# Kernel optimization log

Hardware: AMD Instinct MI355X
Metric: run time of the kernel (lower is better)

Reference implementation:

```python
import jax, jax.numpy as jnp
import numpy as np

NUM_CLASSES = 1000
FEAT_DIM = 512
BATCH = 16384


def setup_inputs() -> dict:
    key = jax.random.key(0)
    k1, k2, k3 = jax.random.split(key, 3)
    x = jax.random.normal(k1, (BATCH, FEAT_DIM), dtype=jnp.float32)
    labels = jax.random.randint(k2, (BATCH,), 0, NUM_CLASSES, dtype=jnp.int64)
    centers = jax.random.normal(k3, (NUM_CLASSES, FEAT_DIM), dtype=jnp.float32)
    margin = jnp.ones((1,), dtype=jnp.float32)
    return {"x": x, "labels": labels, "centers": centers, "margin": margin}


def reference(x, labels, centers, margin):
    # squared euclidean distances: [B, C]
    distmat = (
        jnp.sum(x * x, axis=1, keepdims=True)
        + jnp.sum(centers * centers, axis=1)[None, :]
        - 2.0 * (x @ centers.T)
    )
    B, C = distmat.shape
    onehot = labels[:, None] == jnp.arange(C, dtype=labels.dtype)[None, :]  # [B, C]
    # distance to the true-class center
    dist = jnp.sum(jnp.where(onehot, distmat, 0.0), axis=1)  # [B]
    # min distance over all other classes (mask true class with +inf)
    dist_min = jnp.min(jnp.where(onehot, jnp.inf, distmat), axis=1)  # [B]
    m = margin[0]
    loss = jnp.sum(jnp.maximum(m + dist - dist_min, 0.0)) / B
    return loss
```

## Files before the change

kernel.cpp:

```cpp
#include <hip/hip_runtime.h>
#include <hip/hip_bf16.h>

#define BATCH 16384
#define NCLS  1000
#define NPAD  1024
#define FDIM  512

#define CBLK_STRIDE 266240
#define TAIL_OFF    262144
#define XBLK_STRIDE 262144

typedef __bf16 bf16x8 __attribute__((ext_vector_type(8)));
typedef float  f32x16 __attribute__((ext_vector_type(16)));

#define GLOBAL_AS __attribute__((address_space(1)))
#define LDS_AS    __attribute__((address_space(3)))

#define VMCNT(n) asm volatile("s_waitcnt vmcnt(" #n ")" ::: "memory")
#define LGKM0()  asm volatile("s_waitcnt lgkmcnt(0)" ::: "memory")
#define SBAR()   __builtin_amdgcn_s_barrier()
#define SCHED0() __builtin_amdgcn_sched_barrier(0)

__global__ __launch_bounds__(256) void prep(
    const float* __restrict__ centers, const float* __restrict__ x,
    char* __restrict__ cbt, char* __restrict__ xbt, float* __restrict__ out)
{
    const int bid = blockIdx.x, t = threadIdx.x;
    if (bid == 0 && t == 0) out[0] = 0.f;

    if (bid < 256) {
        const int lane = t & 63;
        const int c = bid * 4 + (t >> 6);
        const int cblk = c >> 8, cl = c & 255;
        char* base = cbt + (size_t)cblk * CBLK_STRIDE;

        float4 f0 = make_float4(0.f, 0.f, 0.f, 0.f);
        float4 f1 = make_float4(0.f, 0.f, 0.f, 0.f);
        if (c < NCLS) {
            f0 = *(const float4*)(centers + (size_t)c * FDIM + lane * 8);
            f1 = *(const float4*)(centers + (size_t)c * FDIM + lane * 8 + 4);
        }
        bf16x8 b;
        b[0] = (__bf16)f0.x; b[1] = (__bf16)f0.y; b[2] = (__bf16)f0.z; b[3] = (__bf16)f0.w;
        b[4] = (__bf16)f1.x; b[5] = (__bf16)f1.y; b[6] = (__bf16)f1.z; b[7] = (__bf16)f1.w;
        *(bf16x8*)(base + (lane >> 3) * 32768 + (lane & 7) * 4096 + cl * 16) = b;

        float ssum = f0.x*f0.x + f0.y*f0.y + f0.z*f0.z + f0.w*f0.w
                   + f1.x*f1.x + f1.y*f1.y + f1.z*f1.z + f1.w*f1.w;
        #pragma unroll
        for (int o = 32; o > 0; o >>= 1) ssum += __shfl_down(ssum, o);
        if (lane == 0) {
            const float hf = (c < NCLS) ? (-0.5f * ssum) : -1e30f;
            const __bf16 h = (__bf16)hf;
            const __bf16 l = (c < NCLS) ? (__bf16)(hf - (float)h) : (__bf16)0.f;
            bf16x8 tl;
            #pragma unroll
            for (int e = 0; e < 8; ++e) tl[e] = (__bf16)0.f;
            tl[0] = h; tl[1] = l;
            *(bf16x8*)(base + TAIL_OFF + cl * 16) = tl;
        }
    } else {
        const int pid  = bid - 256;
        const int bblk = pid >> 3, s = pid & 7;
        const float* src = x + (size_t)(bblk * 256 + t) * FDIM + s * 64;
        float4 f[16];
        #pragma unroll
        for (int j = 0; j < 16; ++j) f[j] = *(const float4*)(src + j * 4);
        char* dst = xbt + (size_t)bblk * XBLK_STRIDE + s * 32768 + t * 16;
        #pragma unroll
        for (int c = 0; c < 8; ++c) {
            bf16x8 b;
            b[0] = (__bf16)f[c*2].x;   b[1] = (__bf16)f[c*2].y;
            b[2] = (__bf16)f[c*2].z;   b[3] = (__bf16)f[c*2].w;
            b[4] = (__bf16)f[c*2+1].x; b[5] = (__bf16)f[c*2+1].y;
            b[6] = (__bf16)f[c*2+1].z; b[7] = (__bf16)f[c*2+1].w;
            *(bf16x8*)(dst + c * 4096) = b;
        }
    }
}

__global__ __launch_bounds__(512, 1) void trip_main(
    const int* __restrict__ labels, const char* __restrict__ cbt,
    const char* __restrict__ xbt, float* __restrict__ mxp,
    float* __restrict__ dap)
{
    extern __shared__ char lds[];
    const int t    = threadIdx.x;
    const int lane = t & 63;
    const int w    = t >> 6;
    const int wN   = w & 3, wM = w >> 2;
    const int l31  = lane & 31, hi = lane >> 5;
    const int bid  = blockIdx.x;
    const int cblk = bid >> 6;
    const int bblk = bid & 63;
    const int class0 = cblk * 256;
    const int row0   = bblk * 256;
    const char* cbB  = cbt + (size_t)cblk * CBLK_STRIDE;
    const char* xbB  = xbt + (size_t)bblk * XBLK_STRIDE;

    auto stageU = [&](int T, int u) {
        const int boff = (T & 1) * 32768 + u * 8192 + t * 16;
        const int goff = T * 32768 + u * 8192 + t * 16;
        __builtin_amdgcn_global_load_lds((const GLOBAL_AS void*)(cbB + goff),
                                         (LDS_AS void*)(lds + boff), 16, 0, 0);
        __builtin_amdgcn_global_load_lds((const GLOBAL_AS void*)(xbB + goff),
                                         (LDS_AS void*)(lds + 65536 + boff), 16, 0, 0);
    };

    f32x16 acc[4][2];
    #pragma unroll
    for (int mi = 0; mi < 4; ++mi)
        #pragma unroll
        for (int ni = 0; ni < 2; ++ni)
            #pragma unroll
            for (int r = 0; r < 16; ++r) acc[mi][ni][r] = 0.f;

    const int lab0 = labels[row0 + wN * 64 + l31];
    const int lab1 = labels[row0 + wN * 64 + 32 + l31];
    SCHED0();
    if (t < 256) {
        const char* src = cbB + TAIL_OFF + t * 16;
        char* dst = lds + 131072 + t * 16;
        __builtin_amdgcn_global_load_lds((const GLOBAL_AS void*)src,
                                         (LDS_AS void*)dst, 16, 0, 0);
    }
    SCHED0();
    stageU(0, 0); SCHED0();
    stageU(0, 1); SCHED0();
    stageU(0, 2); SCHED0();
    stageU(0, 3);
    VMCNT(6);
    SBAR(); SCHED0();

    #pragma unroll
    for (int T = 0; T < 8; ++T) {
        const char* A = lds + (T & 1) * 32768;
        const char* B = lds + 65536 + (T & 1) * 32768;
        #pragma unroll
        for (int u = 0; u < 4; ++u) {
            if (T < 7)          VMCNT(4);
            else if (u == 0)    VMCNT(4);
            else if (u == 1)    VMCNT(2);
            else if (u == 2)    VMCNT(0);
            const int chunk = u * 2 + hi;
            bf16x8 a0 = *(const bf16x8*)(A + chunk * 4096 + (wM * 128 +  0 + l31) * 16);
            bf16x8 a1 = *(const bf16x8*)(A + chunk * 4096 + (wM * 128 + 32 + l31) * 16);
            bf16x8 a2 = *(const bf16x8*)(A + chunk * 4096 + (wM * 128 + 64 + l31) * 16);
            bf16x8 a3 = *(const bf16x8*)(A + chunk * 4096 + (wM * 128 + 96 + l31) * 16);
            bf16x8 b0 = *(const bf16x8*)(B + chunk * 4096 + (wN * 64 +  0 + l31) * 16);
            bf16x8 b1 = *(const bf16x8*)(B + chunk * 4096 + (wN * 64 + 32 + l31) * 16);
            if (T < 7) stageU(T + 1, u);
            SBAR();
            LGKM0();
            SCHED0();
            __builtin_amdgcn_s_setprio(1);
            acc[0][0] = __builtin_amdgcn_mfma_f32_32x32x16_bf16(a0, b0, acc[0][0], 0, 0, 0);
            acc[0][1] = __builtin_amdgcn_mfma_f32_32x32x16_bf16(a0, b1, acc[0][1], 0, 0, 0);
            acc[1][0] = __builtin_amdgcn_mfma_f32_32x32x16_bf16(a1, b0, acc[1][0], 0, 0, 0);
            acc[1][1] = __builtin_amdgcn_mfma_f32_32x32x16_bf16(a1, b1, acc[1][1], 0, 0, 0);
            acc[2][0] = __builtin_amdgcn_mfma_f32_32x32x16_bf16(a2, b0, acc[2][0], 0, 0, 0);
            acc[2][1] = __builtin_amdgcn_mfma_f32_32x32x16_bf16(a2, b1, acc[2][1], 0, 0, 0);
            acc[3][0] = __builtin_amdgcn_mfma_f32_32x32x16_bf16(a3, b0, acc[3][0], 0, 0, 0);
            acc[3][1] = __builtin_amdgcn_mfma_f32_32x32x16_bf16(a3, b1, acc[3][1], 0, 0, 0);
            __builtin_amdgcn_s_setprio(0);
            SBAR();
            SCHED0();
        }
    }

    {
        const char* T = lds + 131072;
        bf16x8 bt;
        #pragma unroll
        for (int e = 0; e < 8; ++e) bt[e] = (__bf16)0.f;
        if (hi == 0) { bt[0] = (__bf16)1.0f; bt[1] = (__bf16)1.0f; }
        #pragma unroll
        for (int mi = 0; mi < 4; ++mi) {
            bf16x8 a = *(const bf16x8*)(T + (wM * 128 + mi * 32 + l31) * 16);
            #pragma unroll
            for (int ni = 0; ni < 2; ++ni)
                acc[mi][ni] = __builtin_amdgcn_mfma_f32_32x32x16_bf16(
                    a, bt, acc[mi][ni], 0, 0, 0);
        }
    }

    const int labBase = class0 + wM * 128 + hi * 4;
    const int labA0 = lab0 - labBase;
    const int labA1 = lab1 - labBase;
    float MX0 = -3e38f, MX1 = -3e38f, DA0 = -3e38f, DA1 = -3e38f;
    #pragma unroll
    for (int mi = 0; mi < 4; ++mi) {
        #pragma unroll
        for (int r = 0; r < 16; ++r) {
            const int pat = mi * 32 + (r & 3) + 8 * (r >> 2);
            {
                const float a = acc[mi][0][r];
                const bool is = (labA0 == pat);
                MX0 = fmaxf(MX0, is ? -3e38f : a);
                DA0 = is ? a : DA0;
            }
            {
                const float a = acc[mi][1][r];
                const bool is = (labA1 == pat);
                MX1 = fmaxf(MX1, is ? -3e38f : a);
                DA1 = is ? a : DA1;
            }
        }
    }
    MX0 = fmaxf(MX0, __shfl_xor(MX0, 32));
    DA0 = fmaxf(DA0, __shfl_xor(DA0, 32));
    MX1 = fmaxf(MX1, __shfl_xor(MX1, 32));
    DA1 = fmaxf(DA1, __shfl_xor(DA1, 32));

    float* sc = (float*)lds;
    const int i0 = (wN * 2 + 0) * 32 + l31;
    const int i1 = (wN * 2 + 1) * 32 + l31;
    __syncthreads();
    if (wM == 1 && hi == 0) {
        sc[i0] = MX0; sc[256 + i0] = DA0;
        sc[i1] = MX1; sc[256 + i1] = DA1;
    }
    __syncthreads();
    if (wM == 0 && hi == 0) {
        const float M0 = fmaxf(MX0, sc[i0]),  D0 = fmaxf(DA0, sc[256 + i0]);
        const float M1 = fmaxf(MX1, sc[i1]),  D1 = fmaxf(DA1, sc[256 + i1]);
        const int rg = row0 + wN * 64 + l31;
        mxp[cblk * BATCH + rg]      = M0;
        dap[cblk * BATCH + rg]      = D0;
        mxp[cblk * BATCH + rg + 32] = M1;
        dap[cblk * BATCH + rg + 32] = D1;
    }
}

__global__ __launch_bounds__(256) void combine(
    const float* __restrict__ mxp, const float* __restrict__ dap,
    const float* __restrict__ margin, float* __restrict__ out)
{
    const int t = threadIdx.x;
    const int row = blockIdx.x * 256 + t;
    float mx = fmaxf(fmaxf(mxp[row], mxp[BATCH + row]),
                     fmaxf(mxp[2 * BATCH + row], mxp[3 * BATCH + row]));
    float da = fmaxf(fmaxf(dap[row], dap[BATCH + row]),
                     fmaxf(dap[2 * BATCH + row], dap[3 * BATCH + row]));
    float loss = fmaxf(margin[0] - 2.f * da + 2.f * mx, 0.f);
    __shared__ float red[4];
    #pragma unroll
    for (int o = 32; o > 0; o >>= 1) loss += __shfl_down(loss, o);
    if ((t & 63) == 0) red[t >> 6] = loss;
    __syncthreads();
    if (t == 0)
        atomicAdd(out, (red[0] + red[1] + red[2] + red[3]) * (1.0f / BATCH));
}

extern "C" void kernel_launch(void* const* d_in, const int* in_sizes, int n_in,
                              void* d_out, int out_size, void* d_ws, size_t ws_size,
                              hipStream_t stream)
{
    const float* x       = (const float*)d_in[0];
    const int*   labels  = (const int*)d_in[1];
    const float* centers = (const float*)d_in[2];
    const float* margin  = (const float*)d_in[3];
    float* out = (float*)d_out;

    char* ws = (char*)d_ws;
    char*  cbt  = ws;
    char*  xbt  = ws + 1064960;
    float* mxp  = (float*)(ws + 17842176);
    float* dap  = (float*)(ws + 18104320);

    (void)hipFuncSetAttribute((const void*)trip_main,
                              hipFuncAttributeMaxDynamicSharedMemorySize, 135168);

    prep<<<768, 256, 0, stream>>>(centers, x, cbt, xbt, out);
    trip_main<<<256, 512, 135168, stream>>>(labels, cbt, xbt, mxp, dap);
    combine<<<64, 256, 0, stream>>>(mxp, dap, margin, out);
}
```

Measured before the change: 33.24 us.

## Load x operand directly into registers, stage only centers through LDS

The x (B) tile is now read with direct global loads into double-buffered register arrays instead of being staged through LDS with global_load_lds. LDS usage roughly halves and the tail block moves down, which cuts LDS traffic and shared-memory footprint. It raises register pressure (16 extra bf16x8 vectors per thread) and changes the vmcnt accounting for the pipeline. Each wave now issues its own uncoalesced-ish global loads for B, and with 256 blocks of 512 threads occupancy likely stays one block per CU.

```diff
diff --git a/kernel.cpp b/kernel.cpp
--- a/kernel.cpp
+++ b/kernel.cpp
@@ -98,13 +98,11 @@
     const char* cbB  = cbt + (size_t)cblk * CBLK_STRIDE;
     const char* xbB  = xbt + (size_t)bblk * XBLK_STRIDE;
 
-    auto stageU = [&](int T, int u) {
-        const int boff = (T & 1) * 32768 + u * 8192 + t * 16;
-        const int goff = T * 32768 + u * 8192 + t * 16;
-        __builtin_amdgcn_global_load_lds((const GLOBAL_AS void*)(cbB + goff),
-                                         (LDS_AS void*)(lds + boff), 16, 0, 0);
-        __builtin_amdgcn_global_load_lds((const GLOBAL_AS void*)(xbB + goff),
-                                         (LDS_AS void*)(lds + 65536 + boff), 16, 0, 0);
+    auto stageAu = [&](int T, int u) {
+        const int off = u * 8192 + t * 16;
+        __builtin_amdgcn_global_load_lds(
+            (const GLOBAL_AS void*)(cbB + T * 32768 + off),
+            (LDS_AS void*)(lds + (T & 1) * 32768 + off), 16, 0, 0);
     };
 
     f32x16 acc[4][2];
@@ -115,53 +113,62 @@
             #pragma unroll
             for (int r = 0; r < 16; ++r) acc[mi][ni][r] = 0.f;
 
+    bf16x8 bE[4][2], bO[4][2];
+
     const int lab0 = labels[row0 + wN * 64 + l31];
     const int lab1 = labels[row0 + wN * 64 + 32 + l31];
-    SCHED0();
     if (t < 256) {
         const char* src = cbB + TAIL_OFF + t * 16;
-        char* dst = lds + 131072 + t * 16;
+        char* dst = lds + 65536 + t * 16;
         __builtin_amdgcn_global_load_lds((const GLOBAL_AS void*)src,
                                          (LDS_AS void*)dst, 16, 0, 0);
     }
-    SCHED0();
-    stageU(0, 0); SCHED0();
-    stageU(0, 1); SCHED0();
-    stageU(0, 2); SCHED0();
-    stageU(0, 3);
-    VMCNT(6);
+    #pragma unroll
+    for (int u = 0; u < 4; ++u) stageAu(0, u);
+    #pragma unroll
+    for (int u = 0; u < 4; ++u) {
+        const char* bsrc = xbB + (u * 2 + hi) * 4096 + (wN * 64 + l31) * 16;
+        bE[u][0] = *(const bf16x8*)(bsrc);
+        bE[u][1] = *(const bf16x8*)(bsrc + 512);
+    }
+    VMCNT(0);
     SBAR(); SCHED0();
 
     #pragma unroll
     for (int T = 0; T < 8; ++T) {
         const char* A = lds + (T & 1) * 32768;
-        const char* B = lds + 65536 + (T & 1) * 32768;
+        auto& bCur = (T & 1) ? bO : bE;
+        auto& bNxt = (T & 1) ? bE : bO;
         #pragma unroll
         for (int u = 0; u < 4; ++u) {
-            if (T < 7)          VMCNT(4);
-            else if (u == 0)    VMCNT(4);
-            else if (u == 1)    VMCNT(2);
-            else if (u == 2)    VMCNT(0);
+            if (T < 7)       { VMCNT(6); }
+            else if (u == 0) { VMCNT(6); }
+            else if (u == 1) { VMCNT(3); }
+            else if (u == 2) { VMCNT(0); }
             const int chunk = u * 2 + hi;
             bf16x8 a0 = *(const bf16x8*)(A + chunk * 4096 + (wM * 128 +  0 + l31) * 16);
             bf16x8 a1 = *(const bf16x8*)(A + chunk * 4096 + (wM * 128 + 32 + l31) * 16);
             bf16x8 a2 = *(const bf16x8*)(A + chunk * 4096 + (wM * 128 + 64 + l31) * 16);
             bf16x8 a3 = *(const bf16x8*)(A + chunk * 4096 + (wM * 128 + 96 + l31) * 16);
-            bf16x8 b0 = *(const bf16x8*)(B + chunk * 4096 + (wN * 64 +  0 + l31) * 16);
-            bf16x8 b1 = *(const bf16x8*)(B + chunk * 4096 + (wN * 64 + 32 + l31) * 16);
-            if (T < 7) stageU(T + 1, u);
+            if (T < 7) {
+                stageAu(T + 1, u);
+                const char* bsrc = xbB + (T + 1) * 32768 + chunk * 4096
+                                 + (wN * 64 + l31) * 16;
+                bNxt[u][0] = *(const bf16x8*)(bsrc);
+                bNxt[u][1] = *(const bf16x8*)(bsrc + 512);
+            }
             SBAR();
             LGKM0();
             SCHED0();
             __builtin_amdgcn_s_setprio(1);
-            acc[0][0] = __builtin_amdgcn_mfma_f32_32x32x16_bf16(a0, b0, acc[0][0], 0, 0, 0);
-            acc[0][1] = __builtin_amdgcn_mfma_f32_32x32x16_bf16(a0, b1, acc[0][1], 0, 0, 0);
-            acc[1][0] = __builtin_amdgcn_mfma_f32_32x32x16_bf16(a1, b0, acc[1][0], 0, 0, 0);
-            acc[1][1] = __builtin_amdgcn_mfma_f32_32x32x16_bf16(a1, b1, acc[1][1], 0, 0, 0);
-            acc[2][0] = __builtin_amdgcn_mfma_f32_32x32x16_bf16(a2, b0, acc[2][0], 0, 0, 0);
-            acc[2][1] = __builtin_amdgcn_mfma_f32_32x32x16_bf16(a2, b1, acc[2][1], 0, 0, 0);
-            acc[3][0] = __builtin_amdgcn_mfma_f32_32x32x16_bf16(a3, b0, acc[3][0], 0, 0, 0);
-            acc[3][1] = __builtin_amdgcn_mfma_f32_32x32x16_bf16(a3, b1, acc[3][1], 0, 0, 0);
+            acc[0][0] = __builtin_amdgcn_mfma_f32_32x32x16_bf16(a0, bCur[u][0], acc[0][0], 0, 0, 0);
+            acc[0][1] = __builtin_amdgcn_mfma_f32_32x32x16_bf16(a0, bCur[u][1], acc[0][1], 0, 0, 0);
+            acc[1][0] = __builtin_amdgcn_mfma_f32_32x32x16_bf16(a1, bCur[u][0], acc[1][0], 0, 0, 0);
+            acc[1][1] = __builtin_amdgcn_mfma_f32_32x32x16_bf16(a1, bCur[u][1], acc[1][1], 0, 0, 0);
+            acc[2][0] = __builtin_amdgcn_mfma_f32_32x32x16_bf16(a2, bCur[u][0], acc[2][0], 0, 0, 0);
+            acc[2][1] = __builtin_amdgcn_mfma_f32_32x32x16_bf16(a2, bCur[u][1], acc[2][1], 0, 0, 0);
+            acc[3][0] = __builtin_amdgcn_mfma_f32_32x32x16_bf16(a3, bCur[u][0], acc[3][0], 0, 0, 0);
+            acc[3][1] = __builtin_amdgcn_mfma_f32_32x32x16_bf16(a3, bCur[u][1], acc[3][1], 0, 0, 0);
             __builtin_amdgcn_s_setprio(0);
             SBAR();
             SCHED0();
@@ -169,7 +176,7 @@
     }
 
     {
-        const char* T = lds + 131072;
+        const char* T = lds + 65536;
         bf16x8 bt;
         #pragma unroll
         for (int e = 0; e < 8; ++e) bt[e] = (__bf16)0.f;
@@ -269,9 +276,9 @@
     float* dap  = (float*)(ws + 18104320);
 
     (void)hipFuncSetAttribute((const void*)trip_main,
-                              hipFuncAttributeMaxDynamicSharedMemorySize, 135168);
+                              hipFuncAttributeMaxDynamicSharedMemorySize, 69632);
 
     prep<<<768, 256, 0, stream>>>(centers, x, cbt, xbt, out);
-    trip_main<<<256, 512, 135168, stream>>>(labels, cbt, xbt, mxp, dap);
+    trip_main<<<256, 512, 69632, stream>>>(labels, cbt, xbt, mxp, dap);
     combine<<<64, 256, 0, stream>>>(mxp, dap, margin, out);
 }
```

New measurement: 34.86 us. 1.05x slower.

## Load MFMA operands directly from global into registers, dropping LDS staging

Applied to the files above, without the earlier changes.

The main GEMM kernel no longer stages the center and x tiles through LDS with global_load_lds and barriers. Each wave now loads its bf16 fragments straight from global memory into registers, double-buffered in two phases (X/Y), and keeps only a small static shared array for the final cross-wave reduction. This removes the per-step barriers and the LDS round trip. In exchange, operands shared across waves are fetched redundantly from global/L2, and the only latency hiding left is a two-deep register prefetch.

```diff
diff --git a/kernel.cpp b/kernel.cpp
--- a/kernel.cpp
+++ b/kernel.cpp
@@ -3,7 +3,6 @@
 
 #define BATCH 16384
 #define NCLS  1000
-#define NPAD  1024
 #define FDIM  512
 
 #define CBLK_STRIDE 266240
@@ -12,14 +11,6 @@
 
 typedef __bf16 bf16x8 __attribute__((ext_vector_type(8)));
 typedef float  f32x16 __attribute__((ext_vector_type(16)));
-
-#define GLOBAL_AS __attribute__((address_space(1)))
-#define LDS_AS    __attribute__((address_space(3)))
-
-#define VMCNT(n) asm volatile("s_waitcnt vmcnt(" #n ")" ::: "memory")
-#define LGKM0()  asm volatile("s_waitcnt lgkmcnt(0)" ::: "memory")
-#define SBAR()   __builtin_amdgcn_s_barrier()
-#define SCHED0() __builtin_amdgcn_sched_barrier(0)
 
 __global__ __launch_bounds__(256) void prep(
     const float* __restrict__ centers, const float* __restrict__ x,
@@ -79,12 +70,38 @@
     }
 }
 
+#define LOADPH(p, A0, A1, A2, A3, B0, B1)                                     \
+    do {                                                                      \
+        const char* ap_ = aB + (p) * 8192;                                    \
+        A0 = *(const bf16x8*)(ap_);                                           \
+        A1 = *(const bf16x8*)(ap_ + 512);                                     \
+        A2 = *(const bf16x8*)(ap_ + 1024);                                    \
+        A3 = *(const bf16x8*)(ap_ + 1536);                                    \
+        const char* bp_ = bB + (p) * 8192;                                    \
+        B0 = *(const bf16x8*)(bp_);                                           \
+        B1 = *(const bf16x8*)(bp_ + 512);                                     \
+    } while (0)
+
+#define MFMAPH(A0, A1, A2, A3, B0, B1)                                        \
+    do {                                                                      \
+        __builtin_amdgcn_s_setprio(1);                                        \
+        acc[0][0] = __builtin_amdgcn_mfma_f32_32x32x16_bf16(A0, B0, acc[0][0], 0, 0, 0); \
+        acc[0][1] = __builtin_amdgcn_mfma_f32_32x32x16_bf16(A0, B1, acc[0][1], 0, 0, 0); \
+        acc[1][0] = __builtin_amdgcn_mfma_f32_32x32x16_bf16(A1, B0, acc[1][0], 0, 0, 0); \
+        acc[1][1] = __builtin_amdgcn_mfma_f32_32x32x16_bf16(A1, B1, acc[1][1], 0, 0, 0); \
+        acc[2][0] = __builtin_amdgcn_mfma_f32_32x32x16_bf16(A2, B0, acc[2][0], 0, 0, 0); \
+        acc[2][1] = __builtin_amdgcn_mfma_f32_32x32x16_bf16(A2, B1, acc[2][1], 0, 0, 0); \
+        acc[3][0] = __builtin_amdgcn_mfma_f32_32x32x16_bf16(A3, B0, acc[3][0], 0, 0, 0); \
+        acc[3][1] = __builtin_amdgcn_mfma_f32_32x32x16_bf16(A3, B1, acc[3][1], 0, 0, 0); \
+        __builtin_amdgcn_s_setprio(0);                                        \
+    } while (0)
+
 __global__ __launch_bounds__(512, 1) void trip_main(
     const int* __restrict__ labels, const char* __restrict__ cbt,
     const char* __restrict__ xbt, float* __restrict__ mxp,
     float* __restrict__ dap)
 {
-    extern __shared__ char lds[];
+    __shared__ float sc[512];
     const int t    = threadIdx.x;
     const int lane = t & 63;
     const int w    = t >> 6;
@@ -95,17 +112,11 @@
     const int bblk = bid & 63;
     const int class0 = cblk * 256;
     const int row0   = bblk * 256;
-    const char* cbB  = cbt + (size_t)cblk * CBLK_STRIDE;
-    const char* xbB  = xbt + (size_t)bblk * XBLK_STRIDE;
-
-    auto stageU = [&](int T, int u) {
-        const int boff = (T & 1) * 32768 + u * 8192 + t * 16;
-        const int goff = T * 32768 + u * 8192 + t * 16;
-        __builtin_amdgcn_global_load_lds((const GLOBAL_AS void*)(cbB + goff),
-                                         (LDS_AS void*)(lds + boff), 16, 0, 0);
-        __builtin_amdgcn_global_load_lds((const GLOBAL_AS void*)(xbB + goff),
-                                         (LDS_AS void*)(lds + 65536 + boff), 16, 0, 0);
-    };
+
+    const char* aB = cbt + (size_t)cblk * CBLK_STRIDE
+                   + hi * 4096 + (wM * 128 + l31) * 16;
+    const char* bB = xbt + (size_t)bblk * XBLK_STRIDE
+                   + hi * 4096 + (wN * 64 + l31) * 16;
 
     f32x16 acc[4][2];
     #pragma unroll
@@ -117,71 +128,43 @@
 
     const int lab0 = labels[row0 + wN * 64 + l31];
     const int lab1 = labels[row0 + wN * 64 + 32 + l31];
-    SCHED0();
-    if (t < 256) {
-        const char* src = cbB + TAIL_OFF + t * 16;
-        char* dst = lds + 131072 + t * 16;
-        __builtin_amdgcn_global_load_lds((const GLOBAL_AS void*)src,
-                                         (LDS_AS void*)dst, 16, 0, 0);
-    }
-    SCHED0();
-    stageU(0, 0); SCHED0();
-    stageU(0, 1); SCHED0();
-    stageU(0, 2); SCHED0();
-    stageU(0, 3);
-    VMCNT(6);
-    SBAR(); SCHED0();
-
-    #pragma unroll
-    for (int T = 0; T < 8; ++T) {
-        const char* A = lds + (T & 1) * 32768;
-        const char* B = lds + 65536 + (T & 1) * 32768;
-        #pragma unroll
-        for (int u = 0; u < 4; ++u) {
-            if (T < 7)          VMCNT(4);
-            else if (u == 0)    VMCNT(4);
-            else if (u == 1)    VMCNT(2);
-            else if (u == 2)    VMCNT(0);
-            const int chunk = u * 2 + hi;
-            bf16x8 a0 = *(const bf16x8*)(A + chunk * 4096 + (wM * 128 +  0 + l31) * 16);
-            bf16x8 a1 = *(const bf16x8*)(A + chunk * 4096 + (wM * 128 + 32 + l31) * 16);
-            bf16x8 a2 = *(const bf16x8*)(A + chunk * 4096 + (wM * 128 + 64 + l31) * 16);
-            bf16x8 a3 = *(const bf16x8*)(A + chunk * 4096 + (wM * 128 + 96 + l31) * 16);
-            bf16x8 b0 = *(const bf16x8*)(B + chunk * 4096 + (wN * 64 +  0 + l31) * 16);
-            bf16x8 b1 = *(const bf16x8*)(B + chunk * 4096 + (wN * 64 + 32 + l31) * 16);
-            if (T < 7) stageU(T + 1, u);
-            SBAR();
-            LGKM0();
-            SCHED0();
-            __builtin_amdgcn_s_setprio(1);
-            acc[0][0] = __builtin_amdgcn_mfma_f32_32x32x16_bf16(a0, b0, acc[0][0], 0, 0, 0);
-            acc[0][1] = __builtin_amdgcn_mfma_f32_32x32x16_bf16(a0, b1, acc[0][1], 0, 0, 0);
-            acc[1][0] = __builtin_amdgcn_mfma_f32_32x32x16_bf16(a1, b0, acc[1][0], 0, 0, 0);
-            acc[1][1] = __builtin_amdgcn_mfma_f32_32x32x16_bf16(a1, b1, acc[1][1], 0, 0, 0);
-            acc[2][0] = __builtin_amdgcn_mfma_f32_32x32x16_bf16(a2, b0, acc[2][0], 0, 0, 0);
-            acc[2][1] = __builtin_amdgcn_mfma_f32_32x32x16_bf16(a2, b1, acc[2][1], 0, 0, 0);
-            acc[3][0] = __builtin_amdgcn_mfma_f32_32x32x16_bf16(a3, b0, acc[3][0], 0, 0, 0);
-            acc[3][1] = __builtin_amdgcn_mfma_f32_32x32x16_bf16(a3, b1, acc[3][1], 0, 0, 0);
-            __builtin_amdgcn_s_setprio(0);
-            SBAR();
-            SCHED0();
-        }
-    }
-
+
+    bf16x8 at0, at1, at2, at3;
     {
-        const char* T = lds + 131072;
+        const char* ts = cbt + (size_t)cblk * CBLK_STRIDE + TAIL_OFF
+                       + (wM * 128 + l31) * 16;
+        at0 = *(const bf16x8*)(ts);
+        at1 = *(const bf16x8*)(ts + 512);
+        at2 = *(const bf16x8*)(ts + 1024);
+        at3 = *(const bf16x8*)(ts + 1536);
+    }
+
+    bf16x8 aX0, aX1, aX2, aX3, bX0, bX1;
+    bf16x8 aY0, aY1, aY2, aY3, bY0, bY1;
+    LOADPH(0, aX0, aX1, aX2, aX3, bX0, bX1);
+    LOADPH(1, aY0, aY1, aY2, aY3, bY0, bY1);
+
+    #pragma unroll
+    for (int q = 0; q < 16; ++q) {
+        MFMAPH(aX0, aX1, aX2, aX3, bX0, bX1);
+        if (2 * q + 2 < 32) LOADPH(2 * q + 2, aX0, aX1, aX2, aX3, bX0, bX1);
+        MFMAPH(aY0, aY1, aY2, aY3, bY0, bY1);
+        if (2 * q + 3 < 32) LOADPH(2 * q + 3, aY0, aY1, aY2, aY3, bY0, bY1);
+    }
+
+    {
         bf16x8 bt;
         #pragma unroll
         for (int e = 0; e < 8; ++e) bt[e] = (__bf16)0.f;
         if (hi == 0) { bt[0] = (__bf16)1.0f; bt[1] = (__bf16)1.0f; }
-        #pragma unroll
-        for (int mi = 0; mi < 4; ++mi) {
-            bf16x8 a = *(const bf16x8*)(T + (wM * 128 + mi * 32 + l31) * 16);
-            #pragma unroll
-            for (int ni = 0; ni < 2; ++ni)
-                acc[mi][ni] = __builtin_amdgcn_mfma_f32_32x32x16_bf16(
-                    a, bt, acc[mi][ni], 0, 0, 0);
-        }
+        acc[0][0] = __builtin_amdgcn_mfma_f32_32x32x16_bf16(at0, bt, acc[0][0], 0, 0, 0);
+        acc[0][1] = __builtin_amdgcn_mfma_f32_32x32x16_bf16(at0, bt, acc[0][1], 0, 0, 0);
+        acc[1][0] = __builtin_amdgcn_mfma_f32_32x32x16_bf16(at1, bt, acc[1][0], 0, 0, 0);
+        acc[1][1] = __builtin_amdgcn_mfma_f32_32x32x16_bf16(at1, bt, acc[1][1], 0, 0, 0);
+        acc[2][0] = __builtin_amdgcn_mfma_f32_32x32x16_bf16(at2, bt, acc[2][0], 0, 0, 0);
+        acc[2][1] = __builtin_amdgcn_mfma_f32_32x32x16_bf16(at2, bt, acc[2][1], 0, 0, 0);
+        acc[3][0] = __builtin_amdgcn_mfma_f32_32x32x16_bf16(at3, bt, acc[3][0], 0, 0, 0);
+        acc[3][1] = __builtin_amdgcn_mfma_f32_32x32x16_bf16(at3, bt, acc[3][1], 0, 0, 0);
     }
 
     const int labBase = class0 + wM * 128 + hi * 4;
@@ -212,18 +195,24 @@
     MX1 = fmaxf(MX1, __shfl_xor(MX1, 32));
     DA1 = fmaxf(DA1, __shfl_xor(DA1, 32));
 
-    float* sc = (float*)lds;
     const int i0 = (wN * 2 + 0) * 32 + l31;
     const int i1 = (wN * 2 + 1) * 32 + l31;
-    __syncthreads();
     if (wM == 1 && hi == 0) {
         sc[i0] = MX0; sc[256 + i0] = DA0;
+    }
+    __syncthreads();
+    float M0 = 0.f, D0 = 0.f;
+    if (wM == 0 && hi == 0) {
+        M0 = fmaxf(MX0, sc[i0]);  D0 = fmaxf(DA0, sc[256 + i0]);
+    }
+    __syncthreads();
+    if (wM == 1 && hi == 0) {
         sc[i1] = MX1; sc[256 + i1] = DA1;
     }
     __syncthreads();
     if (wM == 0 && hi == 0) {
-        const float M0 = fmaxf(MX0, sc[i0]),  D0 = fmaxf(DA0, sc[256 + i0]);
-        const float M1 = fmaxf(MX1, sc[i1]),  D1 = fmaxf(DA1, sc[256 + i1]);
+        const float M1 = fmaxf(MX1, sc[i1]);
+        const float D1 = fmaxf(DA1, sc[256 + i1]);
         const int rg = row0 + wN * 64 + l31;
         mxp[cblk * BATCH + rg]      = M0;
         dap[cblk * BATCH + rg]      = D0;
@@ -268,10 +257,7 @@
     float* mxp  = (float*)(ws + 17842176);
     float* dap  = (float*)(ws + 18104320);
 
-    (void)hipFuncSetAttribute((const void*)trip_main,
-                              hipFuncAttributeMaxDynamicSharedMemorySize, 135168);
-
     prep<<<768, 256, 0, stream>>>(centers, x, cbt, xbt, out);
-    trip_main<<<256, 512, 135168, stream>>>(labels, cbt, xbt, mxp, dap);
+    trip_main<<<256, 512, 0, stream>>>(labels, cbt, xbt, mxp, dap);
     combine<<<64, 256, 0, stream>>>(mxp, dap, margin, out);
 }
```

Measured after the change: 37.18 us. 1.12x slower.
